# Kernel optimization log

Measured on AMD Instinct MI355X. Metric: run time of the kernel, lower is better.

The kernel has to match this reference:

```python
import jax, jax.numpy as jnp
from jax import lax
import numpy as np
from functools import partial

B, N, T, H, L = 16, 256, 4, 128, 2
VOCAB, OUT_VOCAB, MAX_STEPS = 1000, 1000, 15


def setup_inputs() -> dict:
    key = jax.random.key(0)
    ks = jax.random.split(key, 13)
    data = jax.random.randint(ks[0], (B, N, T), 0, VOCAB)
    true_branch_nodes = jax.random.randint(ks[1], (B, N), 0, N)
    false_branch_nodes = jax.random.randint(ks[2], (B, N), 0, N)
    exit_index = jax.random.randint(ks[3], (B,), 0, N)
    steps = jax.random.randint(ks[4], (B,), 1, MAX_STEPS + 1)
    s_in = 1.0 / np.sqrt(H)
    s_cat = 1.0 / np.sqrt(2 * L * H)
    embed = jax.random.uniform(ks[5], (VOCAB, H), jnp.float32, -0.1, 0.1)
    Wi = jax.random.normal(ks[6], (L, H, 4 * H), jnp.float32) * s_in
    Wh = jax.random.normal(ks[7], (L, H, 4 * H), jnp.float32) * s_in
    b_lstm = jnp.zeros((L, 4 * H), jnp.float32)
    Wb = jax.random.normal(ks[8], (2 * L * H, 2), jnp.float32) * s_cat
    bb = jax.random.normal(ks[9], (2,), jnp.float32) * 1e-6
    Wo = jax.random.normal(ks[10], (2 * L * H, OUT_VOCAB), jnp.float32) * s_cat
    bo = jax.random.normal(ks[11], (OUT_VOCAB,), jnp.float32) * 1e-6
    return dict(data=data, true_branch_nodes=true_branch_nodes,
                false_branch_nodes=false_branch_nodes, exit_index=exit_index,
                steps=steps, embed=embed, Wi=Wi, Wh=Wh, b_lstm=b_lstm,
                Wb=Wb, bb=bb, Wo=Wo, bo=bo)


def _lstm_step(Wi_l, Wh_l, b_l, c, h, x):
    # flax LSTMCell math: gates from input (no bias) + recurrent (bias)
    z = x @ Wi_l + h @ Wh_l + b_l  # [..., 4H]
    i, f, g, o = jnp.split(z, 4, axis=-1)
    c2 = jax.nn.sigmoid(f) * c + jax.nn.sigmoid(i) * jnp.tanh(g)
    h2 = jax.nn.sigmoid(o) * jnp.tanh(c2)
    return c2, h2


def _forward(data, true_branch_nodes, false_branch_nodes, exit_index, steps,
             embed, Wi, Wh, b_lstm, Wb, bb, Wo, bo):
    emb = embed[data]                       # [B, N, T, H]
    cs = jnp.zeros((L, B, N, H), embed.dtype)
    hs = jnp.zeros((L, B, N, H), embed.dtype)
    ip = jnp.zeros((B, N), embed.dtype).at[:, 0].set(1.0)
    b_idx = jnp.arange(B)

    seg_b = jax.vmap(partial(jax.ops.segment_sum, num_segments=N))        # [B,N,...] , [B,N]
    seg_lb = jax.vmap(seg_b, in_axes=(0, None))                           # [L,B,N,H]

    def execute(cs, hs):
        # run the stacked LSTM over the T statement tokens at every node
        def tok_step(carry, x_t):
            cs, hs = carry
            inp = x_t
            nc, nh = [], []
            for l in range(L):
                c2, h2 = _lstm_step(Wi[l], Wh[l], b_lstm[l], cs[l], hs[l], inp)
                nc.append(c2); nh.append(h2)
                inp = h2
            return (jnp.stack(nc), jnp.stack(nh)), None
        (cs, hs), _ = lax.scan(tok_step, (cs, hs), jnp.moveaxis(emb, 2, 0))
        return cs, hs

    def step(carry, _):
        cs, hs, ip, idx = carry
        cs_c, hs_c = execute(cs, hs)
        # exit node keeps its previous hidden state
        cs_c = cs_c.at[:, b_idx, exit_index].set(cs[:, b_idx, exit_index])
        hs_c = hs_c.at[:, b_idx, exit_index].set(hs[:, b_idx, exit_index])
        # branch decision from concatenated (c, h) of every layer: [B, N, 2LH]
        feats = jnp.concatenate([x for l in range(L) for x in (cs_c[l], hs_c[l])], axis=-1)
        branch = jax.nn.softmax(feats @ Wb + bb, axis=-1)
        wt = branch[..., 0] * ip            # [B, N]
        wf = branch[..., 1] * ip
        ip_new = seg_b(wt, true_branch_nodes) + seg_b(wf, false_branch_nodes)
        denom = (ip_new + 1e-7)[None, :, :, None]
        def agg(h):
            return (seg_lb(h * wt[None, :, :, None], true_branch_nodes)
                    + seg_lb(h * wf[None, :, :, None], false_branch_nodes)) / denom
        cs_new, hs_new = agg(cs_c), agg(hs_c)
        live = idx < steps                   # [B]
        cs = jnp.where(live[None, :, None, None], cs_new, cs)
        hs = jnp.where(live[None, :, None, None], hs_new, hs)
        ip = jnp.where(live[:, None], ip_new, ip)
        return (cs, hs, ip, idx + 1), None

    (cs, hs, ip, _), _ = lax.scan(step, (cs, hs, ip, jnp.zeros((), jnp.int32)),
                                  None, length=MAX_STEPS)
    fc = cs[:, b_idx, exit_index]           # [L, B, H]
    fh = hs[:, b_idx, exit_index]
    final = jnp.concatenate([x for l in range(L) for x in (fc[l], fh[l])], axis=-1)
    logits = final @ Wo + bo                # [B, OUT_VOCAB]
    return logits[:, None, :]


def reference(data, true_branch_nodes, false_branch_nodes, exit_index, steps,
              embed, Wi, Wh, b_lstm, Wb, bb, Wo, bo):
    return _forward(data, true_branch_nodes, false_branch_nodes, exit_index,
                    steps, embed, Wi, Wh, b_lstm, Wb, bb, Wo, bo)
```

## Files before the change

### kernel.cpp

```cpp
#include <hip/hip_runtime.h>
#include <hip/hip_bf16.h>
#include <stdint.h>
#include <stddef.h>

static constexpr int BB = 16, NN = 256, TT = 4, HH = 128;
static constexpr int MM = BB * NN;
static constexpr int CC = 512;
static constexpr int OUTV = 1000;
static constexpr int MAXS = 15;
static constexpr int SP = 132;

typedef float f32x4 __attribute__((ext_vector_type(4)));
typedef short s16x8 __attribute__((ext_vector_type(8)));

__device__ __forceinline__ float sigf(float x) { return 1.0f / (1.0f + __expf(-x)); }
__device__ __forceinline__ float tanhr(float x) { return 2.0f / (1.0f + __expf(-2.0f * x)) - 1.0f; }
__device__ __forceinline__ unsigned short f2bu(float a) {
  return __builtin_bit_cast(unsigned short, __float2bfloat16(a));
}
__device__ __forceinline__ unsigned int packh(float a, float b) {
  return (unsigned int)f2bu(a) | ((unsigned int)f2bu(b) << 16);
}
__device__ __forceinline__ float blo(unsigned int u) { return __builtin_bit_cast(float, u << 16); }
__device__ __forceinline__ float bhi(unsigned int u) { return __builtin_bit_cast(float, u & 0xffff0000u); }


__global__ __launch_bounds__(512) void csr_kernel(const int* __restrict__ tb,
                                                  const int* __restrict__ fb,
                                                  int* __restrict__ offs,
                                                  int* __restrict__ edges) {
  const int blk = blockIdx.x;
  const int tid = threadIdx.x;
  __shared__ int cnt[256], sc[256], cur[256];
  if (tid < 256) cnt[tid] = 0;
  __syncthreads();
  const int n = tid >> 1, bit = tid & 1;
  const int tgt = bit ? fb[blk * NN + n] : tb[blk * NN + n];
  atomicAdd(&cnt[tgt], 1);
  __syncthreads();
  if (tid < 256) sc[tid] = cnt[tid];
  __syncthreads();
  for (int ofs = 1; ofs < 256; ofs <<= 1) {
    int t2 = (tid < 256 && tid >= ofs) ? sc[tid - ofs] : 0;
    __syncthreads();
    if (tid < 256) sc[tid] += t2;
    __syncthreads();
  }
  if (tid < 256) { offs[blk * NN + tid] = blk * 2 * NN + sc[tid] - cnt[tid]; cur[tid] = 0; }
  if (blk == 0 && tid == 0) offs[MM] = 2 * MM;
  __syncthreads();
  int lpos = sc[tgt] - cnt[tgt] + atomicAdd(&cur[tgt], 1);
  edges[blk * 2 * NN + lpos] = (n << 1) | bit;
}

__global__ __launch_bounds__(256) void prep_kernel(
    const float* __restrict__ Wh0, const float* __restrict__ Wi1, const float* __restrict__ Wh1,
    const float* __restrict__ embed, const float* __restrict__ Wi0, const float* __restrict__ b0,
    unsigned short* __restrict__ swz, float* __restrict__ tab) {
  const int blk = blockIdx.x;
  const int tid = threadIdx.x;
  if (blk < 768) {
    int i = blk * 256 + tid;
    int mtx = i >> 16, ii = i & 65535;
    const float* W = (mtx == 0) ? Wh0 : (mtx == 1) ? Wi1 : Wh1;
    int j = ii & 7, ln = (ii >> 3) & 63, kb = (ii >> 9) & 3, ct = ii >> 11;
    int n = ln & 15, q = ln >> 4;
    swz[i] = f2bu(W[(kb * 32 + q * 8 + j) * CC + ct * 16 + n]);
    return;
  }
  const int v0 = (blk - 768) * 8;
  __shared__ float A[8][HH];
  for (int s = tid; s < 8 * HH; s += 256) {
    int r = s >> 7, k = s & 127;
    A[r][k] = embed[(size_t)(v0 + r) * HH + k];
  }
  __syncthreads();
  const int j = tid;
  float za[8], zb[8];
  {
    float ba = b0[j], bbv = b0[j + 256];
#pragma unroll
    for (int r = 0; r < 8; ++r) { za[r] = ba; zb[r] = bbv; }
  }
#pragma unroll 4
  for (int k = 0; k < HH; ++k) {
    float wa = Wi0[k * CC + j], wb = Wi0[k * CC + j + 256];
#pragma unroll
    for (int r = 0; r < 8; ++r) { za[r] += A[r][k] * wa; zb[r] += A[r][k] * wb; }
  }
#pragma unroll
  for (int r = 0; r < 8; ++r) {
    tab[(size_t)(v0 + r) * CC + j] = za[r];
    tab[(size_t)(v0 + r) * CC + j + 256] = zb[r];
  }
}


__global__ __launch_bounds__(512) void step_kernel(
    float* __restrict__ Sc0g, float* __restrict__ Sh0g,
    float* __restrict__ Sc1g, float* __restrict__ Sh1g,
    const unsigned int* __restrict__ Pr, unsigned int* __restrict__ Pw,
    const float* __restrict__ wtR, const float* __restrict__ wfR,
    float* __restrict__ wtW, float* __restrict__ wfW,
    const int* __restrict__ offs, const int* __restrict__ edges,
    const float* __restrict__ tab,
    const unsigned short* __restrict__ swzWh0, const unsigned short* __restrict__ swzWi1,
    const unsigned short* __restrict__ swzWh1, const float* __restrict__ b1,
    const float* __restrict__ Wb, const float* __restrict__ bb,
    const int* __restrict__ data, const int* __restrict__ exi,
    const int* __restrict__ steps, int step) {
  const int B = blockIdx.x;
  const int b = (B & 7) | (((B >> 3) & 1) << 3);
  const int g16 = B >> 4;
  const int row0 = b * NN + g16 * 16;
  const int sb = steps[b];
  const bool aggLive = (step >= 1) && ((step - 1) < sb);
  const bool lstmLive = (step < sb);
  if (!aggLive && !lstmLive) return;

  const int tid = threadIdx.x;
  const int w = tid >> 6;
  const int lane = tid & 63;
  const int n16 = lane & 15, qq = lane >> 4;
  const int kcol = w * 16 + n16;
  const int basePos = ((kcol >> 5) * 64 + ((kcol >> 3) & 3) * 16) * 8 + (kcol & 7);

  __shared__ float c0L[16 * SP], h0L[16 * SP], c1L[16 * SP], h1L[16 * SP];
  __shared__ __align__(16) unsigned short hA0[2][2048], hA1[2][2048];
  __shared__ float exitP[512];
  __shared__ float ipL[16];
  __shared__ int toks[64];

  s16x8 B0f[4][4], B1f[4][4];
  float b1v[4];
  const s16x8* pWh0 = (const s16x8*)swzWh0;
  const s16x8* pWh1 = (const s16x8*)swzWh1;
  const s16x8* pWi1 = (const s16x8*)swzWi1;
  if (lstmLive) {
#pragma unroll
    for (int g = 0; g < 4; ++g) {
      int ci = w + 8 * g;
#pragma unroll
      for (int kb = 0; kb < 4; ++kb) {
        B0f[g][kb] = pWh0[(ci * 4 + kb) * 64 + lane];
        B1f[g][kb] = pWh1[(ci * 4 + kb) * 64 + lane];
      }
      b1v[g] = b1[ci * 16 + n16];
    }
    if (tid < 64) toks[tid] = data[(row0 + (tid >> 2)) * TT + (tid & 3)];
  }

  if (aggLive) {
    const int l = tid & 31;
    const int m = tid >> 5;
    const int node = row0 + m;
    const int beg = offs[node], end = offs[node + 1];
    float ac0[4] = {0,0,0,0}, ah0[4] = {0,0,0,0}, ac1[4] = {0,0,0,0}, ah1[4] = {0,0,0,0};
    float wsum = 0.f;
    for (int e = beg; e < end; ++e) {
      int rec = edges[e];
      int src = (b << 8) + (rec >> 1);
      float wv = (rec & 1) ? wfR[src] : wtR[src];
      wsum += wv;
      const uint4* pr = (const uint4*)(Pr + (size_t)src * 256 + 8 * l);
      uint4 u0 = pr[0], u1 = pr[1];
      ac0[0] += wv * blo(u0.x); ac0[1] += wv * bhi(u0.x);
      ac0[2] += wv * blo(u0.y); ac0[3] += wv * bhi(u0.y);
      ah0[0] += wv * blo(u0.z); ah0[1] += wv * bhi(u0.z);
      ah0[2] += wv * blo(u0.w); ah0[3] += wv * bhi(u0.w);
      ac1[0] += wv * blo(u1.x); ac1[1] += wv * bhi(u1.x);
      ac1[2] += wv * blo(u1.y); ac1[3] += wv * bhi(u1.y);
      ah1[0] += wv * blo(u1.z); ah1[1] += wv * bhi(u1.z);
      ah1[2] += wv * blo(u1.w); ah1[3] += wv * bhi(u1.w);
    }
    float inv = 1.0f / (wsum + 1e-7f);
    float4 o0 = { ac0[0]*inv, ac0[1]*inv, ac0[2]*inv, ac0[3]*inv };
    float4 o1 = { ah0[0]*inv, ah0[1]*inv, ah0[2]*inv, ah0[3]*inv };
    float4 o2 = { ac1[0]*inv, ac1[1]*inv, ac1[2]*inv, ac1[3]*inv };
    float4 o3 = { ah1[0]*inv, ah1[1]*inv, ah1[2]*inv, ah1[3]*inv };
    ((float4*)c0L)[m * (SP / 4) + l] = o0;
    ((float4*)h0L)[m * (SP / 4) + l] = o1;
    ((float4*)c1L)[m * (SP / 4) + l] = o2;
    ((float4*)h1L)[m * (SP / 4) + l] = o3;
    if (l == 0) ipL[m] = wsum;
    if (!lstmLive) {
      ((float4*)Sc0g)[node * 32 + l] = o0;
      ((float4*)Sh0g)[node * 32 + l] = o1;
      ((float4*)Sc1g)[node * 32 + l] = o2;
      ((float4*)Sh1g)[node * 32 + l] = o3;
    }
  } else {
    for (int i2 = tid; i2 < 16 * HH; i2 += 512) {
      int m = i2 >> 7, k = i2 & 127;
      c0L[m * SP + k] = 0.f; h0L[m * SP + k] = 0.f;
      c1L[m * SP + k] = 0.f; h1L[m * SP + k] = 0.f;
    }
    if (tid < 16) ipL[tid] = (((row0 + tid) & (NN - 1)) == 0) ? 1.0f : 0.0f;
  }
  if (!lstmLive) return;

  const int exnode = exi[b];
  const int exm = exnode - (g16 * 16);
  __syncthreads();

  if (exm >= 0 && exm < 16 && tid < 128) {
    exitP[tid] = c0L[exm * SP + tid];
    exitP[128 + tid] = h0L[exm * SP + tid];
    exitP[256 + tid] = c1L[exm * SP + tid];
    exitP[384 + tid] = h1L[exm * SP + tid];
  }

  float c0r[4], c1r[4], h0r[4], h1r[4];
#pragma unroll
  for (int r = 0; r < 4; ++r) {
    int m = qq * 4 + r;
    c0r[r] = c0L[m * SP + kcol];
    c1r[r] = c1L[m * SP + kcol];
    h0r[r] = h0L[m * SP + kcol];
    h1r[r] = h1L[m * SP + kcol];
    hA0[0][basePos + m * 8] = f2bu(h0r[r]);
    hA1[0][basePos + m * 8] = f2bu(h1r[r]);
  }
  __syncthreads();

  int cur = 0;
  for (int t = 0; t < TT; ++t) {
    const int nxt = cur ^ 1;
    const s16x8* hA0c = (const s16x8*)hA0[cur];
    const s16x8* hA1c = (const s16x8*)hA1[cur];
    s16x8 a0[4], a1b[4];
#pragma unroll
    for (int kb = 0; kb < 4; ++kb) { a0[kb] = hA0c[kb * 64 + lane]; a1b[kb] = hA1c[kb * 64 + lane]; }
    f32x4 d0[4];
#pragma unroll
    for (int g = 0; g < 4; ++g) {
      int colz = (w + 8 * g) * 16 + n16;
#pragma unroll
      for (int r = 0; r < 4; ++r)
        d0[g][r] = tab[(size_t)toks[(qq * 4 + r) * 4 + t] * CC + colz];
    }

#pragma unroll
    for (int g = 0; g < 4; ++g)
#pragma unroll
      for (int kb = 0; kb < 4; ++kb)
        d0[g] = __builtin_amdgcn_mfma_f32_16x16x32_bf16(a0[kb], B0f[g][kb], d0[g], 0, 0, 0);

#pragma unroll
    for (int r = 0; r < 4; ++r) {
      float cn = sigf(d0[1][r]) * c0r[r] + sigf(d0[0][r]) * tanhr(d0[2][r]);
      float hn = sigf(d0[3][r]) * tanhr(cn);
      c0r[r] = cn; h0r[r] = hn;
      hA0[nxt][basePos + (qq * 4 + r) * 8] = f2bu(hn);
    }
    __syncthreads();

    const s16x8* hA0n = (const s16x8*)hA0[nxt];
    s16x8 a1a[4];
#pragma unroll
    for (int kb = 0; kb < 4; ++kb) a1a[kb] = hA0n[kb * 64 + lane];
    f32x4 d1[4];
#pragma unroll
    for (int g = 0; g < 4; ++g) {
      int ci = w + 8 * g;
      s16x8 wi[4];
#pragma unroll
      for (int kb = 0; kb < 4; ++kb) wi[kb] = pWi1[(ci * 4 + kb) * 64 + lane];
      f32x4 d = { b1v[g], b1v[g], b1v[g], b1v[g] };
#pragma unroll
      for (int kb = 0; kb < 4; ++kb)
        d = __builtin_amdgcn_mfma_f32_16x16x32_bf16(a1a[kb], wi[kb], d, 0, 0, 0);
#pragma unroll
      for (int kb = 0; kb < 4; ++kb)
        d = __builtin_amdgcn_mfma_f32_16x16x32_bf16(a1b[kb], B1f[g][kb], d, 0, 0, 0);
      d1[g] = d;
    }

#pragma unroll
    for (int r = 0; r < 4; ++r) {
      float cn = sigf(d1[1][r]) * c1r[r] + sigf(d1[0][r]) * tanhr(d1[2][r]);
      float hn = sigf(d1[3][r]) * tanhr(cn);
      c1r[r] = cn; h1r[r] = hn;
      hA1[nxt][basePos + (qq * 4 + r) * 8] = f2bu(hn);
    }
    __syncthreads();
    cur = nxt;
  }

#pragma unroll
  for (int r = 0; r < 4; ++r) {
    int m = qq * 4 + r;
    c0L[m * SP + kcol] = c0r[r];
    h0L[m * SP + kcol] = h0r[r];
    c1L[m * SP + kcol] = c1r[r];
    h1L[m * SP + kcol] = h1r[r];
  }
  __syncthreads();

  {
    const int m = tid >> 5, sub = tid & 31;
    const int row = row0 + m;
    const bool isExit = (m == exm);
    float z0 = 0.f, z1 = 0.f;
#pragma unroll
    for (int u = 0; u < 16; ++u) {
      int k = u * 32 + sub;
      int seg = k >> 7, kk = k & 127;
      float fk;
      if (isExit) {
        fk = exitP[seg * 128 + kk];
      } else {
        fk = (seg == 0) ? c0L[m * SP + kk] : (seg == 1) ? h0L[m * SP + kk]
           : (seg == 2) ? c1L[m * SP + kk] : h1L[m * SP + kk];
      }
      z0 += fk * Wb[2 * k];
      z1 += fk * Wb[2 * k + 1];
    }
#pragma unroll
    for (int off = 16; off >= 1; off >>= 1) {
      z0 += __shfl_xor(z0, off);
      z1 += __shfl_xor(z1, off);
    }
    if (sub == 0) {
      z0 += bb[0]; z1 += bb[1];
      float mx = fmaxf(z0, z1);
      float e0 = __expf(z0 - mx), e1 = __expf(z1 - mx);
      float inv = 1.0f / (e0 + e1);
      float ipv = ipL[m];
      wtW[row] = e0 * inv * ipv;
      wfW[row] = e1 * inv * ipv;
    }
  }

  {
    const int m = tid >> 5, l = tid & 31;
    const bool ex = (m == exm);
    const int grow = row0 + m;
    float f0[4], f1[4], f2[4], f3[4];
#pragma unroll
    for (int i = 0; i < 4; ++i) {
      int k = 4 * l + i;
      f0[i] = ex ? exitP[k] : c0L[m * SP + k];
      f1[i] = ex ? exitP[128 + k] : h0L[m * SP + k];
      f2[i] = ex ? exitP[256 + k] : c1L[m * SP + k];
      f3[i] = ex ? exitP[384 + k] : h1L[m * SP + k];
    }
    uint4 o0 = { packh(f0[0], f0[1]), packh(f0[2], f0[3]),
                 packh(f1[0], f1[1]), packh(f1[2], f1[3]) };
    uint4 o1 = { packh(f2[0], f2[1]), packh(f2[2], f2[3]),
                 packh(f3[0], f3[1]), packh(f3[2], f3[3]) };
    uint4* pw = (uint4*)(Pw + (size_t)grow * 256 + 8 * l);
    pw[0] = o0; pw[1] = o1;
  }
}

__global__ void final_kernel(const float* __restrict__ Sc0, const float* __restrict__ Sh0,
                             const float* __restrict__ Sc1, const float* __restrict__ Sh1,
                             const int* __restrict__ exi, const float* __restrict__ Wo,
                             const float* __restrict__ bo, float* __restrict__ out) {
  const int b = blockIdx.x >> 2;
  const int vt = blockIdx.x & 3;
  const int tid = threadIdx.x;
  __shared__ float f[512];
  int row = b * NN + exi[b];
  if (tid < 128) {
    size_t g = (size_t)row * HH + tid;
    f[tid] = Sc0[g];
    f[128 + tid] = Sh0[g];
    f[256 + tid] = Sc1[g];
    f[384 + tid] = Sh1[g];
  }
  __syncthreads();
  if (tid < 250) {
    int v = vt * 250 + tid;
    float acc = bo[v];
#pragma unroll 8
    for (int k = 0; k < 512; ++k) acc += f[k] * Wo[(size_t)k * OUTV + v];
    out[b * OUTV + v] = acc;
  }
}

__global__ void zero_out_kernel(float* __restrict__ out, int n) {
  int i = blockIdx.x * blockDim.x + threadIdx.x;
  if (i < n) out[i] = 0.0f;
}


extern "C" void kernel_launch(void* const* d_in, const int* in_sizes, int n_in,
                              void* d_out, int out_size, void* d_ws, size_t ws_size,
                              hipStream_t stream) {
  const int* data = (const int*)d_in[0];
  const int* tb   = (const int*)d_in[1];
  const int* fb   = (const int*)d_in[2];
  const int* exi  = (const int*)d_in[3];
  const int* steps = (const int*)d_in[4];
  const float* embed = (const float*)d_in[5];
  const float* Wi = (const float*)d_in[6];
  const float* Wh = (const float*)d_in[7];
  const float* bl = (const float*)d_in[8];
  const float* Wb = (const float*)d_in[9];
  const float* bb = (const float*)d_in[10];
  const float* Wo = (const float*)d_in[11];
  const float* bo = (const float*)d_in[12];
  float* out = (float*)d_out;

  const float* Wi0 = Wi;
  const float* Wi1 = Wi + HH * CC;
  const float* Wh0 = Wh;
  const float* Wh1 = Wh + HH * CC;
  const float* b0 = bl;
  const float* b1 = bl + CC;

  float* ws = (float*)d_ws;
  size_t off = 0;
  float* tab = ws + off;  off += (size_t)1024 * CC;
  float* Sc0 = ws + off;  off += (size_t)MM * HH;
  float* Sh0 = ws + off;  off += (size_t)MM * HH;
  float* Sc1 = ws + off;  off += (size_t)MM * HH;
  float* Sh1 = ws + off;  off += (size_t)MM * HH;
  unsigned int* PA = (unsigned int*)(ws + off); off += (size_t)MM * 256;
  unsigned int* PB = (unsigned int*)(ws + off); off += (size_t)MM * 256;
  unsigned short* swz = (unsigned short*)(ws + off); off += 3 * 32768;
  float* wtA = ws + off;  off += MM;
  float* wfA = ws + off;  off += MM;
  float* wtB = ws + off;  off += MM;
  float* wfB = ws + off;  off += MM;
  int* offs  = (int*)(ws + off); off += MM + 16;
  int* edges = (int*)(ws + off); off += 2 * MM;
  (void)in_sizes; (void)n_in; (void)out_size;

  if (ws_size < off * sizeof(float)) {
    zero_out_kernel<<<(BB * OUTV + 255) / 256, 256, 0, stream>>>(out, BB * OUTV);
    return;
  }

  unsigned short* swzWh0 = swz;
  unsigned short* swzWi1 = swz + 65536;
  unsigned short* swzWh1 = swz + 2 * 65536;

  csr_kernel<<<BB, 512, 0, stream>>>(tb, fb, offs, edges);
  prep_kernel<<<893, 256, 0, stream>>>(Wh0, Wi1, Wh1, embed, Wi0, b0, swz, tab);

  for (int s = 0; s <= MAXS; ++s) {
    unsigned int* Pwp = (s & 1) ? PB : PA;
    const unsigned int* Prp = (s & 1) ? PA : PB;
    float* wtWp = (s & 1) ? wtB : wtA;
    float* wfWp = (s & 1) ? wfB : wfA;
    const float* wtRp = (s & 1) ? wtA : wtB;
    const float* wfRp = (s & 1) ? wfA : wfB;
    step_kernel<<<MM / 16, 512, 0, stream>>>(
        Sc0, Sh0, Sc1, Sh1, Prp, Pwp,
        wtRp, wfRp, wtWp, wfWp,
        offs, edges, tab, swzWh0, swzWi1, swzWh1, b1, Wb, bb,
        data, exi, steps, s);
  }
  final_kernel<<<BB * 4, 256, 0, stream>>>(Sc0, Sh0, Sc1, Sh1, exi, Wo, bo, out);
}
```

Baseline: 552.9 us.

## Fuse per-step launches into one persistent kernel with per-batch spin barriers

Replaces the sixteen step_kernel launches with a single persistent kernel of 256 blocks. Each batch's 16 blocks synchronise through a global atomic counter: they spin with s_sleep and fall back to a timeout. Weight fragments and the block's CSR edge list are loaded into registers and LDS once instead of every step. This removes launch overhead and repeated setup, but it depends on all 256 blocks being co-resident. If a block cannot become resident, the timeout break lets the others read stale data silently.

```diff
diff --git a/kernel.cpp b/kernel.cpp
--- a/kernel.cpp
+++ b/kernel.cpp
@@ -28,10 +28,12 @@
 __global__ __launch_bounds__(512) void csr_kernel(const int* __restrict__ tb,
                                                   const int* __restrict__ fb,
                                                   int* __restrict__ offs,
-                                                  int* __restrict__ edges) {
+                                                  int* __restrict__ edges,
+                                                  unsigned int* __restrict__ bar) {
   const int blk = blockIdx.x;
   const int tid = threadIdx.x;
   __shared__ int cnt[256], sc[256], cur[256];
+  if (tid == 0) bar[blk] = 0;
   if (tid < 256) cnt[tid] = 0;
   __syncthreads();
   const int n = tid >> 1, bit = tid & 1;
@@ -96,28 +98,24 @@
 }
 
 
-__global__ __launch_bounds__(512) void step_kernel(
+__global__ __launch_bounds__(512) void persist_kernel(
     float* __restrict__ Sc0g, float* __restrict__ Sh0g,
     float* __restrict__ Sc1g, float* __restrict__ Sh1g,
-    const unsigned int* __restrict__ Pr, unsigned int* __restrict__ Pw,
-    const float* __restrict__ wtR, const float* __restrict__ wfR,
-    float* __restrict__ wtW, float* __restrict__ wfW,
+    unsigned int* __restrict__ PA, unsigned int* __restrict__ PB,
+    float* __restrict__ wtA, float* __restrict__ wfA,
+    float* __restrict__ wtB, float* __restrict__ wfB,
     const int* __restrict__ offs, const int* __restrict__ edges,
     const float* __restrict__ tab,
     const unsigned short* __restrict__ swzWh0, const unsigned short* __restrict__ swzWi1,
     const unsigned short* __restrict__ swzWh1, const float* __restrict__ b1,
     const float* __restrict__ Wb, const float* __restrict__ bb,
     const int* __restrict__ data, const int* __restrict__ exi,
-    const int* __restrict__ steps, int step) {
-  const int B = blockIdx.x;
-  const int b = (B & 7) | (((B >> 3) & 1) << 3);
-  const int g16 = B >> 4;
+    const int* __restrict__ steps, unsigned int* __restrict__ bar) {
+  const int Bk = blockIdx.x;
+  const int b = Bk & 15;
+  const int g16 = Bk >> 4;
   const int row0 = b * NN + g16 * 16;
   const int sb = steps[b];
-  const bool aggLive = (step >= 1) && ((step - 1) < sb);
-  const bool lstmLive = (step < sb);
-  if (!aggLive && !lstmLive) return;
-
   const int tid = threadIdx.x;
   const int w = tid >> 6;
   const int lane = tid & 63;
@@ -130,227 +128,262 @@
   __shared__ float exitP[512];
   __shared__ float ipL[16];
   __shared__ int toks[64];
+  __shared__ int edgeL[512];
 
   s16x8 B0f[4][4], B1f[4][4];
   float b1v[4];
   const s16x8* pWh0 = (const s16x8*)swzWh0;
   const s16x8* pWh1 = (const s16x8*)swzWh1;
   const s16x8* pWi1 = (const s16x8*)swzWi1;
-  if (lstmLive) {
-#pragma unroll
-    for (int g = 0; g < 4; ++g) {
-      int ci = w + 8 * g;
-#pragma unroll
-      for (int kb = 0; kb < 4; ++kb) {
-        B0f[g][kb] = pWh0[(ci * 4 + kb) * 64 + lane];
-        B1f[g][kb] = pWh1[(ci * 4 + kb) * 64 + lane];
-      }
-      b1v[g] = b1[ci * 16 + n16];
-    }
-    if (tid < 64) toks[tid] = data[(row0 + (tid >> 2)) * TT + (tid & 3)];
-  }
-
-  if (aggLive) {
-    const int l = tid & 31;
-    const int m = tid >> 5;
-    const int node = row0 + m;
-    const int beg = offs[node], end = offs[node + 1];
-    float ac0[4] = {0,0,0,0}, ah0[4] = {0,0,0,0}, ac1[4] = {0,0,0,0}, ah1[4] = {0,0,0,0};
-    float wsum = 0.f;
-    for (int e = beg; e < end; ++e) {
-      int rec = edges[e];
-      int src = (b << 8) + (rec >> 1);
-      float wv = (rec & 1) ? wfR[src] : wtR[src];
-      wsum += wv;
-      const uint4* pr = (const uint4*)(Pr + (size_t)src * 256 + 8 * l);
-      uint4 u0 = pr[0], u1 = pr[1];
-      ac0[0] += wv * blo(u0.x); ac0[1] += wv * bhi(u0.x);
-      ac0[2] += wv * blo(u0.y); ac0[3] += wv * bhi(u0.y);
-      ah0[0] += wv * blo(u0.z); ah0[1] += wv * bhi(u0.z);
-      ah0[2] += wv * blo(u0.w); ah0[3] += wv * bhi(u0.w);
-      ac1[0] += wv * blo(u1.x); ac1[1] += wv * bhi(u1.x);
-      ac1[2] += wv * blo(u1.y); ac1[3] += wv * bhi(u1.y);
-      ah1[0] += wv * blo(u1.z); ah1[1] += wv * bhi(u1.z);
-      ah1[2] += wv * blo(u1.w); ah1[3] += wv * bhi(u1.w);
-    }
-    float inv = 1.0f / (wsum + 1e-7f);
-    float4 o0 = { ac0[0]*inv, ac0[1]*inv, ac0[2]*inv, ac0[3]*inv };
-    float4 o1 = { ah0[0]*inv, ah0[1]*inv, ah0[2]*inv, ah0[3]*inv };
-    float4 o2 = { ac1[0]*inv, ac1[1]*inv, ac1[2]*inv, ac1[3]*inv };
-    float4 o3 = { ah1[0]*inv, ah1[1]*inv, ah1[2]*inv, ah1[3]*inv };
-    ((float4*)c0L)[m * (SP / 4) + l] = o0;
-    ((float4*)h0L)[m * (SP / 4) + l] = o1;
-    ((float4*)c1L)[m * (SP / 4) + l] = o2;
-    ((float4*)h1L)[m * (SP / 4) + l] = o3;
-    if (l == 0) ipL[m] = wsum;
-    if (!lstmLive) {
-      ((float4*)Sc0g)[node * 32 + l] = o0;
-      ((float4*)Sh0g)[node * 32 + l] = o1;
-      ((float4*)Sc1g)[node * 32 + l] = o2;
-      ((float4*)Sh1g)[node * 32 + l] = o3;
-    }
-  } else {
-    for (int i2 = tid; i2 < 16 * HH; i2 += 512) {
-      int m = i2 >> 7, k = i2 & 127;
-      c0L[m * SP + k] = 0.f; h0L[m * SP + k] = 0.f;
-      c1L[m * SP + k] = 0.f; h1L[m * SP + k] = 0.f;
-    }
-    if (tid < 16) ipL[tid] = (((row0 + tid) & (NN - 1)) == 0) ? 1.0f : 0.0f;
-  }
-  if (!lstmLive) return;
+#pragma unroll
+  for (int g = 0; g < 4; ++g) {
+    int ci = w + 8 * g;
+#pragma unroll
+    for (int kb = 0; kb < 4; ++kb) {
+      B0f[g][kb] = pWh0[(ci * 4 + kb) * 64 + lane];
+      B1f[g][kb] = pWh1[(ci * 4 + kb) * 64 + lane];
+    }
+    b1v[g] = b1[ci * 16 + n16];
+  }
+  if (tid < 64) toks[tid] = data[(row0 + (tid >> 2)) * TT + (tid & 3)];
+
+  const int beg0 = offs[row0];
+  const int ecnt = offs[row0 + 16] - beg0;
+  for (int i = tid; i < ecnt; i += 512) edgeL[i] = edges[beg0 + i];
 
   const int exnode = exi[b];
   const int exm = exnode - (g16 * 16);
-  __syncthreads();
-
-  if (exm >= 0 && exm < 16 && tid < 128) {
-    exitP[tid] = c0L[exm * SP + tid];
-    exitP[128 + tid] = h0L[exm * SP + tid];
-    exitP[256 + tid] = c1L[exm * SP + tid];
-    exitP[384 + tid] = h1L[exm * SP + tid];
-  }
-
-  float c0r[4], c1r[4], h0r[4], h1r[4];
-#pragma unroll
-  for (int r = 0; r < 4; ++r) {
-    int m = qq * 4 + r;
-    c0r[r] = c0L[m * SP + kcol];
-    c1r[r] = c1L[m * SP + kcol];
-    h0r[r] = h0L[m * SP + kcol];
-    h1r[r] = h1L[m * SP + kcol];
-    hA0[0][basePos + m * 8] = f2bu(h0r[r]);
-    hA1[0][basePos + m * 8] = f2bu(h1r[r]);
-  }
-  __syncthreads();
-
-  int cur = 0;
-  for (int t = 0; t < TT; ++t) {
-    const int nxt = cur ^ 1;
-    const s16x8* hA0c = (const s16x8*)hA0[cur];
-    const s16x8* hA1c = (const s16x8*)hA1[cur];
-    s16x8 a0[4], a1b[4];
-#pragma unroll
-    for (int kb = 0; kb < 4; ++kb) { a0[kb] = hA0c[kb * 64 + lane]; a1b[kb] = hA1c[kb * 64 + lane]; }
-    f32x4 d0[4];
-#pragma unroll
-    for (int g = 0; g < 4; ++g) {
-      int colz = (w + 8 * g) * 16 + n16;
-#pragma unroll
-      for (int r = 0; r < 4; ++r)
-        d0[g][r] = tab[(size_t)toks[(qq * 4 + r) * 4 + t] * CC + colz];
-    }
-
-#pragma unroll
-    for (int g = 0; g < 4; ++g)
-#pragma unroll
-      for (int kb = 0; kb < 4; ++kb)
-        d0[g] = __builtin_amdgcn_mfma_f32_16x16x32_bf16(a0[kb], B0f[g][kb], d0[g], 0, 0, 0);
-
+  const bool isExitBlk = (exm >= 0 && exm < 16);
+
+  const int gl = tid & 31;
+  const int gm = tid >> 5;
+  const int gnode = row0 + gm;
+  const int gbeg = offs[gnode] - beg0;
+  const int gend = offs[gnode + 1] - beg0;
+
+  unsigned int* barb = bar + b;
+  __syncthreads();
+
+  for (int s = 0; s <= MAXS; ++s) {
+    const unsigned int* Pr = (s & 1) ? PA : PB;
+    unsigned int* Pw = (s & 1) ? PB : PA;
+    const float* wtR = (s & 1) ? wtA : wtB;
+    const float* wfR = (s & 1) ? wfA : wfB;
+    float* wtW = (s & 1) ? wtB : wtA;
+    float* wfW = (s & 1) ? wfB : wfA;
+    const bool lstmLive = (s < sb);
+
+    if (s > 0) {
+      if (tid == 0) {
+        const unsigned int tgt = 16u * (unsigned int)s;
+        unsigned long long t0 = __builtin_amdgcn_s_memrealtime();
+        while (__hip_atomic_load(barb, __ATOMIC_RELAXED, __HIP_MEMORY_SCOPE_AGENT) < tgt) {
+          __builtin_amdgcn_s_sleep(8);
+          if (__builtin_amdgcn_s_memrealtime() - t0 > 500000ull) break;
+        }
+        (void)__hip_atomic_load(barb, __ATOMIC_ACQUIRE, __HIP_MEMORY_SCOPE_AGENT);
+      }
+      __syncthreads();
+
+      float ac0[4] = {0,0,0,0}, ah0[4] = {0,0,0,0}, ac1[4] = {0,0,0,0}, ah1[4] = {0,0,0,0};
+      float wsum = 0.f;
+      for (int e = gbeg; e < gend; ++e) {
+        int rec = edgeL[e];
+        int src = (b << 8) + (rec >> 1);
+        float wv = (rec & 1) ? wfR[src] : wtR[src];
+        wsum += wv;
+        const uint4* pr = (const uint4*)(Pr + (size_t)src * 256 + 8 * gl);
+        uint4 u0 = pr[0], u1 = pr[1];
+        ac0[0] += wv * blo(u0.x); ac0[1] += wv * bhi(u0.x);
+        ac0[2] += wv * blo(u0.y); ac0[3] += wv * bhi(u0.y);
+        ah0[0] += wv * blo(u0.z); ah0[1] += wv * bhi(u0.z);
+        ah0[2] += wv * blo(u0.w); ah0[3] += wv * bhi(u0.w);
+        ac1[0] += wv * blo(u1.x); ac1[1] += wv * bhi(u1.x);
+        ac1[2] += wv * blo(u1.y); ac1[3] += wv * bhi(u1.y);
+        ah1[0] += wv * blo(u1.z); ah1[1] += wv * bhi(u1.z);
+        ah1[2] += wv * blo(u1.w); ah1[3] += wv * bhi(u1.w);
+      }
+      float inv = 1.0f / (wsum + 1e-7f);
+      float4 o0 = { ac0[0]*inv, ac0[1]*inv, ac0[2]*inv, ac0[3]*inv };
+      float4 o1 = { ah0[0]*inv, ah0[1]*inv, ah0[2]*inv, ah0[3]*inv };
+      float4 o2 = { ac1[0]*inv, ac1[1]*inv, ac1[2]*inv, ac1[3]*inv };
+      float4 o3 = { ah1[0]*inv, ah1[1]*inv, ah1[2]*inv, ah1[3]*inv };
+      ((float4*)c0L)[gm * (SP / 4) + gl] = o0;
+      ((float4*)h0L)[gm * (SP / 4) + gl] = o1;
+      ((float4*)c1L)[gm * (SP / 4) + gl] = o2;
+      ((float4*)h1L)[gm * (SP / 4) + gl] = o3;
+      if (gl == 0) ipL[gm] = wsum;
+      if (!lstmLive) {
+        ((float4*)Sc0g)[gnode * 32 + gl] = o0;
+        ((float4*)Sh0g)[gnode * 32 + gl] = o1;
+        ((float4*)Sc1g)[gnode * 32 + gl] = o2;
+        ((float4*)Sh1g)[gnode * 32 + gl] = o3;
+        break;
+      }
+    } else {
+      for (int i2 = tid; i2 < 16 * HH; i2 += 512) {
+        int m = i2 >> 7, k = i2 & 127;
+        c0L[m * SP + k] = 0.f; h0L[m * SP + k] = 0.f;
+        c1L[m * SP + k] = 0.f; h1L[m * SP + k] = 0.f;
+      }
+      if (tid < 16) ipL[tid] = (((row0 + tid) & (NN - 1)) == 0) ? 1.0f : 0.0f;
+    }
+
+    __syncthreads();
+
+    if (isExitBlk && tid < 128) {
+      exitP[tid] = c0L[exm * SP + tid];
+      exitP[128 + tid] = h0L[exm * SP + tid];
+      exitP[256 + tid] = c1L[exm * SP + tid];
+      exitP[384 + tid] = h1L[exm * SP + tid];
+    }
+
+    float c0r[4], c1r[4], h0r[4], h1r[4];
 #pragma unroll
     for (int r = 0; r < 4; ++r) {
-      float cn = sigf(d0[1][r]) * c0r[r] + sigf(d0[0][r]) * tanhr(d0[2][r]);
-      float hn = sigf(d0[3][r]) * tanhr(cn);
-      c0r[r] = cn; h0r[r] = hn;
-      hA0[nxt][basePos + (qq * 4 + r) * 8] = f2bu(hn);
-    }
-    __syncthreads();
-
-    const s16x8* hA0n = (const s16x8*)hA0[nxt];
-    s16x8 a1a[4];
-#pragma unroll
-    for (int kb = 0; kb < 4; ++kb) a1a[kb] = hA0n[kb * 64 + lane];
-    f32x4 d1[4];
-#pragma unroll
-    for (int g = 0; g < 4; ++g) {
-      int ci = w + 8 * g;
-      s16x8 wi[4];
-#pragma unroll
-      for (int kb = 0; kb < 4; ++kb) wi[kb] = pWi1[(ci * 4 + kb) * 64 + lane];
-      f32x4 d = { b1v[g], b1v[g], b1v[g], b1v[g] };
-#pragma unroll
-      for (int kb = 0; kb < 4; ++kb)
-        d = __builtin_amdgcn_mfma_f32_16x16x32_bf16(a1a[kb], wi[kb], d, 0, 0, 0);
-#pragma unroll
-      for (int kb = 0; kb < 4; ++kb)
-        d = __builtin_amdgcn_mfma_f32_16x16x32_bf16(a1b[kb], B1f[g][kb], d, 0, 0, 0);
-      d1[g] = d;
+      int m = qq * 4 + r;
+      c0r[r] = c0L[m * SP + kcol];
+      c1r[r] = c1L[m * SP + kcol];
+      h0r[r] = h0L[m * SP + kcol];
+      h1r[r] = h1L[m * SP + kcol];
+      hA0[0][basePos + m * 8] = f2bu(h0r[r]);
+      hA1[0][basePos + m * 8] = f2bu(h1r[r]);
+    }
+    __syncthreads();
+
+    int cur = 0;
+    for (int t = 0; t < TT; ++t) {
+      const int nxt = cur ^ 1;
+      const s16x8* hA0c = (const s16x8*)hA0[cur];
+      const s16x8* hA1c = (const s16x8*)hA1[cur];
+      s16x8 a0[4], a1b[4];
+#pragma unroll
+      for (int kb = 0; kb < 4; ++kb) { a0[kb] = hA0c[kb * 64 + lane]; a1b[kb] = hA1c[kb * 64 + lane]; }
+      f32x4 d0[4];
+#pragma unroll
+      for (int g = 0; g < 4; ++g) {
+        int colz = (w + 8 * g) * 16 + n16;
+#pragma unroll
+        for (int r = 0; r < 4; ++r)
+          d0[g][r] = tab[(size_t)toks[(qq * 4 + r) * 4 + t] * CC + colz];
+      }
+
+#pragma unroll
+      for (int g = 0; g < 4; ++g)
+#pragma unroll
+        for (int kb = 0; kb < 4; ++kb)
+          d0[g] = __builtin_amdgcn_mfma_f32_16x16x32_bf16(a0[kb], B0f[g][kb], d0[g], 0, 0, 0);
+
+#pragma unroll
+      for (int r = 0; r < 4; ++r) {
+        float cn = sigf(d0[1][r]) * c0r[r] + sigf(d0[0][r]) * tanhr(d0[2][r]);
+        float hn = sigf(d0[3][r]) * tanhr(cn);
+        c0r[r] = cn; h0r[r] = hn;
+        hA0[nxt][basePos + (qq * 4 + r) * 8] = f2bu(hn);
+      }
+      __syncthreads();
+
+      const s16x8* hA0n = (const s16x8*)hA0[nxt];
+      s16x8 a1a[4];
+#pragma unroll
+      for (int kb = 0; kb < 4; ++kb) a1a[kb] = hA0n[kb * 64 + lane];
+      f32x4 d1[4];
+#pragma unroll
+      for (int g = 0; g < 4; ++g) {
+        int ci = w + 8 * g;
+        s16x8 wi[4];
+#pragma unroll
+        for (int kb = 0; kb < 4; ++kb) wi[kb] = pWi1[(ci * 4 + kb) * 64 + lane];
+        f32x4 d = { b1v[g], b1v[g], b1v[g], b1v[g] };
+#pragma unroll
+        for (int kb = 0; kb < 4; ++kb)
+          d = __builtin_amdgcn_mfma_f32_16x16x32_bf16(a1a[kb], wi[kb], d, 0, 0, 0);
+#pragma unroll
+        for (int kb = 0; kb < 4; ++kb)
+          d = __builtin_amdgcn_mfma_f32_16x16x32_bf16(a1b[kb], B1f[g][kb], d, 0, 0, 0);
+        d1[g] = d;
+      }
+
+#pragma unroll
+      for (int r = 0; r < 4; ++r) {
+        float cn = sigf(d1[1][r]) * c1r[r] + sigf(d1[0][r]) * tanhr(d1[2][r]);
+        float hn = sigf(d1[3][r]) * tanhr(cn);
+        c1r[r] = cn; h1r[r] = hn;
+        hA1[nxt][basePos + (qq * 4 + r) * 8] = f2bu(hn);
+      }
+      __syncthreads();
+      cur = nxt;
     }
 
 #pragma unroll
     for (int r = 0; r < 4; ++r) {
-      float cn = sigf(d1[1][r]) * c1r[r] + sigf(d1[0][r]) * tanhr(d1[2][r]);
-      float hn = sigf(d1[3][r]) * tanhr(cn);
-      c1r[r] = cn; h1r[r] = hn;
-      hA1[nxt][basePos + (qq * 4 + r) * 8] = f2bu(hn);
-    }
-    __syncthreads();
-    cur = nxt;
-  }
-
-#pragma unroll
-  for (int r = 0; r < 4; ++r) {
-    int m = qq * 4 + r;
-    c0L[m * SP + kcol] = c0r[r];
-    h0L[m * SP + kcol] = h0r[r];
-    c1L[m * SP + kcol] = c1r[r];
-    h1L[m * SP + kcol] = h1r[r];
-  }
-  __syncthreads();
-
-  {
-    const int m = tid >> 5, sub = tid & 31;
-    const int row = row0 + m;
-    const bool isExit = (m == exm);
-    float z0 = 0.f, z1 = 0.f;
-#pragma unroll
-    for (int u = 0; u < 16; ++u) {
-      int k = u * 32 + sub;
-      int seg = k >> 7, kk = k & 127;
-      float fk;
-      if (isExit) {
-        fk = exitP[seg * 128 + kk];
-      } else {
-        fk = (seg == 0) ? c0L[m * SP + kk] : (seg == 1) ? h0L[m * SP + kk]
-           : (seg == 2) ? c1L[m * SP + kk] : h1L[m * SP + kk];
-      }
-      z0 += fk * Wb[2 * k];
-      z1 += fk * Wb[2 * k + 1];
-    }
-#pragma unroll
-    for (int off = 16; off >= 1; off >>= 1) {
-      z0 += __shfl_xor(z0, off);
-      z1 += __shfl_xor(z1, off);
-    }
-    if (sub == 0) {
-      z0 += bb[0]; z1 += bb[1];
-      float mx = fmaxf(z0, z1);
-      float e0 = __expf(z0 - mx), e1 = __expf(z1 - mx);
-      float inv = 1.0f / (e0 + e1);
-      float ipv = ipL[m];
-      wtW[row] = e0 * inv * ipv;
-      wfW[row] = e1 * inv * ipv;
-    }
-  }
-
-  {
-    const int m = tid >> 5, l = tid & 31;
-    const bool ex = (m == exm);
-    const int grow = row0 + m;
-    float f0[4], f1[4], f2[4], f3[4];
-#pragma unroll
-    for (int i = 0; i < 4; ++i) {
-      int k = 4 * l + i;
-      f0[i] = ex ? exitP[k] : c0L[m * SP + k];
-      f1[i] = ex ? exitP[128 + k] : h0L[m * SP + k];
-      f2[i] = ex ? exitP[256 + k] : c1L[m * SP + k];
-      f3[i] = ex ? exitP[384 + k] : h1L[m * SP + k];
-    }
-    uint4 o0 = { packh(f0[0], f0[1]), packh(f0[2], f0[3]),
-                 packh(f1[0], f1[1]), packh(f1[2], f1[3]) };
-    uint4 o1 = { packh(f2[0], f2[1]), packh(f2[2], f2[3]),
-                 packh(f3[0], f3[1]), packh(f3[2], f3[3]) };
-    uint4* pw = (uint4*)(Pw + (size_t)grow * 256 + 8 * l);
-    pw[0] = o0; pw[1] = o1;
+      int m = qq * 4 + r;
+      c0L[m * SP + kcol] = c0r[r];
+      h0L[m * SP + kcol] = h0r[r];
+      c1L[m * SP + kcol] = c1r[r];
+      h1L[m * SP + kcol] = h1r[r];
+    }
+    __syncthreads();
+
+    {
+      const int m = tid >> 5, sub = tid & 31;
+      const int row = row0 + m;
+      const bool isExit = (m == exm);
+      float z0 = 0.f, z1 = 0.f;
+#pragma unroll
+      for (int u = 0; u < 16; ++u) {
+        int k = u * 32 + sub;
+        int seg = k >> 7, kk = k & 127;
+        float fk;
+        if (isExit) {
+          fk = exitP[seg * 128 + kk];
+        } else {
+          fk = (seg == 0) ? c0L[m * SP + kk] : (seg == 1) ? h0L[m * SP + kk]
+             : (seg == 2) ? c1L[m * SP + kk] : h1L[m * SP + kk];
+        }
+        z0 += fk * Wb[2 * k];
+        z1 += fk * Wb[2 * k + 1];
+      }
+#pragma unroll
+      for (int off2 = 16; off2 >= 1; off2 >>= 1) {
+        z0 += __shfl_xor(z0, off2);
+        z1 += __shfl_xor(z1, off2);
+      }
+      if (sub == 0) {
+        z0 += bb[0]; z1 += bb[1];
+        float mx = fmaxf(z0, z1);
+        float e0 = __expf(z0 - mx), e1 = __expf(z1 - mx);
+        float inv2 = 1.0f / (e0 + e1);
+        float ipv = ipL[m];
+        wtW[row] = e0 * inv2 * ipv;
+        wfW[row] = e1 * inv2 * ipv;
+      }
+    }
+
+    {
+      const int m = tid >> 5, l = tid & 31;
+      const bool ex = (m == exm);
+      const int grow = row0 + m;
+      float f0[4], f1[4], f2[4], f3[4];
+#pragma unroll
+      for (int i = 0; i < 4; ++i) {
+        int k = 4 * l + i;
+        f0[i] = ex ? exitP[k] : c0L[m * SP + k];
+        f1[i] = ex ? exitP[128 + k] : h0L[m * SP + k];
+        f2[i] = ex ? exitP[256 + k] : c1L[m * SP + k];
+        f3[i] = ex ? exitP[384 + k] : h1L[m * SP + k];
+      }
+      uint4 o0 = { packh(f0[0], f0[1]), packh(f0[2], f0[3]),
+                   packh(f1[0], f1[1]), packh(f1[2], f1[3]) };
+      uint4 o1 = { packh(f2[0], f2[1]), packh(f2[2], f2[3]),
+                   packh(f3[0], f3[1]), packh(f3[2], f3[3]) };
+      uint4* pw = (uint4*)(Pw + (size_t)grow * 256 + 8 * l);
+      pw[0] = o0; pw[1] = o1;
+    }
+
+    __syncthreads();
+    if (tid == 0)
+      __hip_atomic_fetch_add(barb, 1u, __ATOMIC_RELEASE, __HIP_MEMORY_SCOPE_AGENT);
   }
 }
 
@@ -427,6 +460,7 @@
   float* wfB = ws + off;  off += MM;
   int* offs  = (int*)(ws + off); off += MM + 16;
   int* edges = (int*)(ws + off); off += 2 * MM;
+  unsigned int* bar = (unsigned int*)(ws + off); off += 16;
   (void)in_sizes; (void)n_in; (void)out_size;
 
   if (ws_size < off * sizeof(float)) {
@@ -438,21 +472,14 @@
   unsigned short* swzWi1 = swz + 65536;
   unsigned short* swzWh1 = swz + 2 * 65536;
 
-  csr_kernel<<<BB, 512, 0, stream>>>(tb, fb, offs, edges);
+  csr_kernel<<<BB, 512, 0, stream>>>(tb, fb, offs, edges, bar);
   prep_kernel<<<893, 256, 0, stream>>>(Wh0, Wi1, Wh1, embed, Wi0, b0, swz, tab);
 
-  for (int s = 0; s <= MAXS; ++s) {
-    unsigned int* Pwp = (s & 1) ? PB : PA;
-    const unsigned int* Prp = (s & 1) ? PA : PB;
-    float* wtWp = (s & 1) ? wtB : wtA;
-    float* wfWp = (s & 1) ? wfB : wfA;
-    const float* wtRp = (s & 1) ? wtA : wtB;
-    const float* wfRp = (s & 1) ? wfA : wfB;
-    step_kernel<<<MM / 16, 512, 0, stream>>>(
-        Sc0, Sh0, Sc1, Sh1, Prp, Pwp,
-        wtRp, wfRp, wtWp, wfWp,
-        offs, edges, tab, swzWh0, swzWi1, swzWh1, b1, Wb, bb,
-        data, exi, steps, s);
-  }
+  persist_kernel<<<MM / 16, 512, 0, stream>>>(
+      Sc0, Sh0, Sc1, Sh1, PA, PB,
+      wtA, wfA, wtB, wfB,
+      offs, edges, tab, swzWh0, swzWi1, swzWh1, b1, Wb, bb,
+      data, exi, steps, bar);
+
   final_kernel<<<BB * 4, 256, 0, stream>>>(Sc0, Sh0, Sc1, Sh1, exi, Wo, bo, out);
 }
```

Result: slower. 1.002 ms (+81.2%).
